# Performance work log

Hardware: AMD Instinct MI355X
Metric: run time of the kernel (lower is better)

The kernel has to match this reference:

```python
import jax, jax.numpy as jnp
import numpy as np

B, N, C, H = 16, 4096, 384, 8
D = C // H  # head_dim = 48
WSTD = 0.02


def setup_inputs() -> dict:
    key = jax.random.key(0)
    ks = jax.random.split(key, 9)
    return {
        "x": jax.random.normal(ks[0], (B, N, C), dtype=jnp.float32),
        "conv_w": jax.random.normal(ks[1], (C, C), dtype=jnp.float32) * WSTD,  # Conv1d k=1, squeezed
        "conv_b": jax.random.normal(ks[2], (C,), dtype=jnp.float32) * WSTD,
        "wq": jax.random.normal(ks[3], (C, C), dtype=jnp.float32) * WSTD,
        "bq": jax.random.normal(ks[4], (C,), dtype=jnp.float32) * WSTD,
        "wkv": jax.random.normal(ks[5], (2 * C, C), dtype=jnp.float32) * WSTD,
        "bkv": jax.random.normal(ks[6], (2 * C,), dtype=jnp.float32) * WSTD,
        "wp": jax.random.normal(ks[7], (C, C), dtype=jnp.float32) * WSTD,
        "bp": jax.random.normal(ks[8], (C,), dtype=jnp.float32) * WSTD,
    }


def reference(x, conv_w, conv_b, wq, bq, wkv, bkv, wp, bp):
    b, n, c = x.shape
    h, d = H, c // H
    # Conv1d kernel_size=1 over channels == per-token linear: y = x @ W^T + b
    x_in = jnp.einsum("bnc,oc->bno", x, conv_w) + conv_b  # [B,N,C]
    # q: reshape(B,N,1,H,d).permute(2,0,3,4,1)[0] -> [B,H,d,N]
    q = (x_in @ wq.T + bq).reshape(b, n, h, d).transpose(0, 2, 3, 1)  # [B,H,d,N]
    kv = (x_in @ wkv.T + bkv).reshape(b, n, 2, h, d).transpose(2, 0, 3, 4, 1)  # [2,B,H,d,N]
    k, v = kv[0], kv[1]
    scale = jnp.asarray(n, x.dtype) ** -0.5  # note: N^-0.5, not head_dim^-0.5
    attn = jax.nn.softmax((q * scale) @ jnp.swapaxes(k, -2, -1), axis=-1)  # [B,H,d,d]
    out = attn @ v  # [B,H,d,N]
    # transpose(1,2) -> [B,d,H,N], then raw reshape to [B,N,C] (verbatim torch layout)
    out = jnp.transpose(out, (0, 2, 1, 3)).reshape(b, n, c)
    return out @ wp.T + bp
```

## Files before the change

### kernel.cpp

```cpp
#include <hip/hip_runtime.h>
#include <hip/hip_bf16.h>
#include <stdint.h>

#define DEVI static __device__ __forceinline__

typedef __attribute__((ext_vector_type(4))) float f32x4;
typedef __attribute__((ext_vector_type(8))) short bf16x8;
typedef unsigned short u16;
typedef unsigned int u32;
typedef unsigned long long u64;

#define BB 16
#define NN 4096
#define CC 384
#define HH 8
#define DD 48

DEVI u16 f2bf(float f) {
  union { float f; u32 u; } c; c.f = f;
  u32 u = c.u;
  u32 r = (u + 0x7FFFu + ((u >> 16) & 1u)) >> 16;
  return (u16)r;
}
DEVI float bf2f(u16 h) {
  union { float f; u32 u; } c; c.u = ((u32)h) << 16;
  return c.f;
}
DEVI void stage8(u16* dst, const float* src) {
  const f32x4 a = *(const f32x4*)(src);
  const f32x4 b = *(const f32x4*)(src + 4);
  union { bf16x8 v; u16 u[8]; } o;
  o.u[0] = f2bf(a[0]); o.u[1] = f2bf(a[1]); o.u[2] = f2bf(a[2]); o.u[3] = f2bf(a[3]);
  o.u[4] = f2bf(b[0]); o.u[5] = f2bf(b[1]); o.u[6] = f2bf(b[2]); o.u[7] = f2bf(b[3]);
  *(bf16x8*)dst = o.v;
}

typedef const __attribute__((address_space(1))) void* gas_ptr;
typedef __attribute__((address_space(3))) void* las_ptr;
DEVI void gload16(const void* g, void* l) {
  __builtin_amdgcn_global_load_lds((gas_ptr)g, (las_ptr)l, 16, 0, 0);
}

__global__ __launch_bounds__(256)
void f32_to_bf16(const float* __restrict__ in, u16* __restrict__ out, int n8) {
  const int i = blockIdx.x * 256 + threadIdx.x;
  if (i >= n8) return;
  u16 tmp[8];
  stage8(tmp, in + (size_t)i * 8);
  *(bf16x8*)(out + (size_t)i * 8) = *(bf16x8*)tmp;
}

__global__ __launch_bounds__(256)
void convert_x(const float* __restrict__ x, u16* __restrict__ xb,
               u16* __restrict__ xbT) {
  __shared__ __align__(8) u16 Lt[64 * 68];
  const int ct = blockIdx.x, nt = blockIdx.y, b = blockIdx.z;
  const int t = threadIdx.x;
  const int n0 = nt * 64, c0 = ct * 64;
#pragma unroll
  for (int it = 0; it < 4; ++it) {
    const int row = it * 16 + (t >> 4), col = (t & 15) * 4;
    const f32x4 v = *(const f32x4*)&x[((size_t)(b * NN + n0 + row)) * CC + c0 + col];
    u64 pk = (u64)f2bf(v[0]) | ((u64)f2bf(v[1]) << 16) |
             ((u64)f2bf(v[2]) << 32) | ((u64)f2bf(v[3]) << 48);
    *(u64*)(&Lt[row * 68 + col]) = pk;
  }
  __syncthreads();
#pragma unroll
  for (int it = 0; it < 2; ++it) {
    const int v = it * 256 + t, row = v >> 3, cg = v & 7;
    union { bf16x8 o; u64 q[2]; } u;
    u.q[0] = *(const u64*)(&Lt[row * 68 + cg * 8]);
    u.q[1] = *(const u64*)(&Lt[row * 68 + cg * 8 + 4]);
    *(bf16x8*)&xb[((size_t)(b * NN + n0 + row)) * CC + c0 + cg * 8] = u.o;
  }
#pragma unroll
  for (int it = 0; it < 2; ++it) {
    const int v = it * 256 + t, c = v >> 3, ng = v & 7;
    union { bf16x8 o; u16 e[8]; } u;
#pragma unroll
    for (int r = 0; r < 8; ++r) u.e[r] = Lt[(ng * 8 + r) * 68 + c];
    *(bf16x8*)&xbT[((size_t)(b * CC + c0 + c)) * NN + n0 + ng * 8] = u.o;
  }
}

__global__ __launch_bounds__(256)
void transpose_cw(const float* __restrict__ cw, u16* __restrict__ cwT) {
  __shared__ __align__(8) u16 Lt[64 * 68];
  const int mt = blockIdx.x, ct = blockIdx.y;
  const int t = threadIdx.x;
  const int m0 = mt * 64, c0 = ct * 64;
#pragma unroll
  for (int it = 0; it < 4; ++it) {
    const int row = it * 16 + (t >> 4), col = (t & 15) * 4;
    const f32x4 v = *(const f32x4*)&cw[(size_t)(m0 + row) * CC + c0 + col];
    u64 pk = (u64)f2bf(v[0]) | ((u64)f2bf(v[1]) << 16) |
             ((u64)f2bf(v[2]) << 32) | ((u64)f2bf(v[3]) << 48);
    *(u64*)(&Lt[row * 68 + col]) = pk;
  }
  __syncthreads();
#pragma unroll
  for (int it = 0; it < 2; ++it) {
    const int v = it * 256 + t, c = v >> 3, mg = v & 7;
    union { bf16x8 o; u16 e[8]; } u;
#pragma unroll
    for (int r = 0; r < 8; ++r) u.e[r] = Lt[(mg * 8 + r) * 68 + c];
    *(bf16x8*)&cwT[(size_t)(c0 + c) * CC + m0 + mg * 8] = u.o;
  }
}

__global__ __launch_bounds__(256)
void bias_fuse(const float* __restrict__ wq, const float* __restrict__ bq,
               const float* __restrict__ wkv, const float* __restrict__ bkv,
               const float* __restrict__ cb, float* __restrict__ bf_) {
  const int o = blockIdx.x * 4 + (threadIdx.x >> 6);
  const int lane = threadIdx.x & 63;
  const float* wrow;
  float b0;
  if (o < CC) { wrow = wq + (size_t)o * CC;        b0 = bq[o]; }
  else        { wrow = wkv + (size_t)(o - CC) * CC; b0 = bkv[o - CC]; }
  float s = 0.f;
  for (int m = lane; m < CC; m += 64) s += wrow[m] * cb[m];
#pragma unroll
  for (int off = 32; off; off >>= 1) s += __shfl_xor(s, off, 64);
  if (lane == 0) bf_[o] = b0 + s;
}

__global__ __launch_bounds__(256)
void colsum(const u16* __restrict__ xbT, float* __restrict__ sx) {
  const int b = blockIdx.y, c = blockIdx.x * 16 + (threadIdx.x >> 4);
  const int sl = threadIdx.x & 15;
  const u16* src = xbT + ((size_t)(b * CC + c)) * NN + sl * 256;
  float s = 0.f;
  for (int i = 0; i < 32; ++i) {
    const bf16x8 v = *(const bf16x8*)(src + i * 8);
#pragma unroll
    for (int r = 0; r < 8; ++r) s += bf2f((u16)v[r]);
  }
#pragma unroll
  for (int m = 1; m < 16; m <<= 1) s += __shfl_xor(s, m, 64);
  if (sl == 0) sx[b * CC + c] = s;
}

__global__ __launch_bounds__(128)
void proj_sx(const u16* __restrict__ Wf, const float* __restrict__ sx,
             float* __restrict__ P) {
  __shared__ float sl[CC];
  const int b = blockIdx.y, o = blockIdx.x * 128 + threadIdx.x;
  for (int i = threadIdx.x; i < CC; i += 128) sl[i] = sx[b * CC + i];
  __syncthreads();
  float acc = 0.f;
  const u16* wr = Wf + (size_t)o * CC;
  for (int c8 = 0; c8 < CC; c8 += 8) {
    const bf16x8 w = *(const bf16x8*)(wr + c8);
#pragma unroll
    for (int r = 0; r < 8; ++r) acc += bf2f((u16)w[r]) * sl[c8 + r];
  }
  P[b * 768 + o] = acc;
}

template<typename OT, int BIASMODE, int TRI = 0, int SWZ = 1>
__global__ __launch_bounds__(256)
void gemm_f(const u16* __restrict__ A, const u16* __restrict__ W,
            const float* __restrict__ bias, OT* __restrict__ C,
            int M, int N, int K, int klen, int nbn, int nbm, int tpb,
            long sA, long sW, long sC, long sCp, long sBias) {
  constexpr int BK = 64;
  __shared__ __align__(16) u16 smem[32768];

  const int nx = gridDim.x;
  const int lin = blockIdx.x;
  const int lin2 = SWZ ? (lin & 7) * (nx >> 3) + (lin >> 3) : lin;
  const int b = lin2 / tpb;
  int t2 = lin2 % tpb;
  int bn, bm, p;
  if constexpr (TRI) {
    const int tl = t2 % 6; p = t2 / 6;
    bm = tl < 3 ? 0 : (tl < 5 ? 1 : 2);
    bn = tl < 3 ? tl : (tl < 5 ? tl - 2 : 2);
  } else {
    bn = t2 % nbn; t2 /= nbn;
    bm = t2 % nbm;
    p = t2 / nbm;
  }
  A += (size_t)b * sA; W += (size_t)b * sW;
  C += (size_t)b * sC + (size_t)p * sCp;
  if (BIASMODE) bias += (size_t)b * sBias;

  const int t = threadIdx.x;
  const int wid = t >> 6, lane = t & 63;
  const int wr = wid >> 1, wc = wid & 1;
  const int row0 = bm * 128, col0 = bn * 128;
  const int lrow = lane & 15;
  const int lswz = (lane & 7) << 3;
  const int kstart = p * klen;

  const int arow = t >> 3;
  const int scol = ((t & 7) ^ ((t >> 3) & 7)) * 8;
  const u16* Ag = A + (size_t)(row0 + arow) * K + scol;
  const u16* Wg = W + (size_t)(col0 + arow) * K + scol;

  f32x4 acc[4][4] = {};
  const int NT = klen >> 6;

  auto stage = [&](int buf, int kt) {
    u16* Al = smem + buf * 16384 + t * 8;
    u16* Bl = smem + buf * 16384 + 8192 + t * 8;
    const int k0 = kstart + kt * BK;
#pragma unroll
    for (int it = 0; it < 4; ++it) {
      gload16(Ag + (size_t)(it * 32) * K + k0, Al + it * 2048);
      gload16(Wg + (size_t)(it * 32) * K + k0, Bl + it * 2048);
    }
  };

  stage(0, 0);
  __syncthreads();
  int cur = 0;
  for (int kt = 0; kt < NT; ++kt) {
    if (kt + 1 < NT) stage(cur ^ 1, kt + 1);
    const u16* As = smem + cur * 16384;
    const u16* Bs = smem + cur * 16384 + 8192;
#pragma unroll
    for (int kk = 0; kk < 2; ++kk) {
      const int lk = (kk * 32 + (lane >> 4) * 8) ^ lswz;
      bf16x8 af[4], bf[4];
#pragma unroll
      for (int i = 0; i < 4; ++i)
        af[i] = *(const bf16x8*)&As[(wr * 64 + i * 16 + lrow) * BK + lk];
#pragma unroll
      for (int j = 0; j < 4; ++j)
        bf[j] = *(const bf16x8*)&Bs[(wc * 64 + j * 16 + lrow) * BK + lk];
#pragma unroll
      for (int i = 0; i < 4; ++i)
#pragma unroll
        for (int j = 0; j < 4; ++j)
          acc[i][j] = __builtin_amdgcn_mfma_f32_16x16x32_bf16(af[i], bf[j], acc[i][j], 0, 0, 0);
    }
    __syncthreads();
    cur ^= 1;
  }

  const int lr = (lane >> 4) * 4;
  if constexpr (sizeof(OT) == 2) {
    u16* Ct = smem;
#pragma unroll
    for (int i = 0; i < 4; ++i)
#pragma unroll
      for (int j = 0; j < 4; ++j) {
        const int ccol = wc * 64 + j * 16 + lrow;
        float bv = 0.f;
        if constexpr (BIASMODE == 1) bv = bias[col0 + ccol];
#pragma unroll
        for (int r = 0; r < 4; ++r) {
          const int rrow = wr * 64 + i * 16 + lr + r;
          float b2 = bv;
          if constexpr (BIASMODE == 2) b2 = bias[row0 + rrow];
          Ct[rrow * 132 + ccol] = f2bf(acc[i][j][r] + b2);
        }
      }
    __syncthreads();
#pragma unroll
    for (int it = 0; it < 8; ++it) {
      const int id = it * 256 + t;
      const int row = id >> 4, c16 = (id & 15) * 8;
      *(bf16x8*)((u16*)C + (size_t)(row0 + row) * N + col0 + c16) =
          *(const bf16x8*)&Ct[row * 132 + c16];
    }
  } else {
    const int orow = row0 + wr * 64, ocol = col0 + wc * 64;
#pragma unroll
    for (int i = 0; i < 4; ++i)
#pragma unroll
      for (int j = 0; j < 4; ++j) {
        const int cc2 = ocol + j * 16 + lrow;
        float bv = 0.f;
        if constexpr (BIASMODE == 1) bv = bias[cc2];
#pragma unroll
        for (int r = 0; r < 4; ++r) {
          const int rr = orow + i * 16 + lr + r;
          float b2 = bv;
          if constexpr (BIASMODE == 2) b2 = bias[rr];
          C[(size_t)rr * N + cc2] = acc[i][j][r] + b2;
        }
      }
  }
}

__global__ __launch_bounds__(256)
void reduceG(const float* __restrict__ Gp, u16* __restrict__ Gbf) {
  const int b = blockIdx.y;
  const int e = blockIdx.x * 256 + threadIdx.x;
  const int i = e / CC, j = e % CC;
  const int ee = (i <= j) ? e : (j * CC + i);
  const float* s = Gp + (size_t)b * 4 * 147456 + ee;
  Gbf[(size_t)b * 147456 + e] =
      f2bf(s[0] + s[147456] + s[2 * 147456] + s[3 * 147456]);
}

__global__ __launch_bounds__(256)
void s_softmax(const u16* __restrict__ M1g, const u16* __restrict__ Wf,
               const float* __restrict__ bf_, const float* __restrict__ P,
               const u16* __restrict__ UvT, u16* __restrict__ AUb,
               float* __restrict__ rbias) {
  __shared__ float Sf[48 * 52];
  __shared__ __align__(16) u16 att[48 * 56];
  const int bh = blockIdx.x, b = bh >> 3, h = bh & 7;
  const int t = threadIdx.x, wid = t >> 6, lane = t & 63;
  const int lrow = lane & 15, lkq = lane >> 4;

  if (wid < 3) {
    f32x4 acc[3] = {};
    const u16* Arow = M1g + (size_t)b * 147456 + (size_t)(h * 48 + wid * 16 + lrow) * CC;
    const u16* Brow = Wf + (size_t)(CC + h * 48) * CC;
    for (int ks = 0; ks < 12; ++ks) {
      const int k = ks * 32 + lkq * 8;
      const bf16x8 af = *(const bf16x8*)(Arow + k);
#pragma unroll
      for (int j = 0; j < 3; ++j) {
        const bf16x8 bfr = *(const bf16x8*)(Brow + (size_t)(j * 16 + lrow) * CC + k);
        acc[j] = __builtin_amdgcn_mfma_f32_16x16x32_bf16(af, bfr, acc[j], 0, 0, 0);
      }
    }
    const int lr = lkq * 4;
#pragma unroll
    for (int j = 0; j < 3; ++j)
#pragma unroll
      for (int r = 0; r < 4; ++r)
        Sf[(wid * 16 + lr + r) * 52 + j * 16 + lrow] = acc[j][r];
  }
  __syncthreads();

  if (t < 48) {
    const float bi = bf_[h * 48 + t];
    const float pq = P[b * 768 + h * 48 + t];
    float row[48];
    float mx = -1e30f;
#pragma unroll
    for (int j = 0; j < 48; ++j) {
      const float g = bf_[CC + h * 48 + j];
      const float pk = P[b * 768 + CC + h * 48 + j];
      const float s = (Sf[t * 52 + j] + bi * pk + pq * g + 4096.f * bi * g) * 0.015625f;
      row[j] = s;
      mx = fmaxf(mx, s);
    }
    float sum = 0.f;
#pragma unroll
    for (int j = 0; j < 48; ++j) { row[j] = __expf(row[j] - mx); sum += row[j]; }
    const float inv = 1.f / sum;
    float rb = 0.f;
#pragma unroll
    for (int j = 0; j < 48; ++j) {
      const float a = row[j] * inv;
      att[t * 56 + j] = f2bf(a);
      rb += a * bf_[2 * CC + h * 48 + j];
    }
#pragma unroll
    for (int j = 48; j < 56; ++j) att[t * 56 + j] = 0;
    rbias[b * CC + t * 8 + h] = rb;
  }
  __syncthreads();

  f32x4 acc[3][6] = {};
  const u16* Vbase = UvT + h * 48;
  const bf16x8 z = {};
#pragma unroll
  for (int kk = 0; kk < 2; ++kk) {
    const int k = kk * 32 + lkq * 8;
    bf16x8 af[3];
#pragma unroll
    for (int i = 0; i < 3; ++i) {
      af[i] = *(const bf16x8*)&att[(i * 16 + lrow) * 56 + k];
      if (k >= 48) af[i] = z;
    }
#pragma unroll
    for (int ct = 0; ct < 6; ++ct) {
      const int c = wid * 96 + ct * 16 + lrow;
      bf16x8 bfr = *(const bf16x8*)(Vbase + (size_t)c * CC + k);
      if (k >= 48) bfr = z;
#pragma unroll
      for (int i = 0; i < 3; ++i)
        acc[i][ct] = __builtin_amdgcn_mfma_f32_16x16x32_bf16(af[i], bfr, acc[i][ct], 0, 0, 0);
    }
  }
  const int lr = lkq * 4;
#pragma unroll
  for (int i = 0; i < 3; ++i)
#pragma unroll
    for (int ct = 0; ct < 6; ++ct) {
      const int c = wid * 96 + ct * 16 + lrow;
#pragma unroll
      for (int r = 0; r < 4; ++r) {
        const int ii = i * 16 + lr + r;
        AUb[(size_t)b * 147456 + (size_t)(ii * 8 + h) * CC + c] = f2bf(acc[i][ct][r]);
      }
    }
}

extern "C" void kernel_launch(void* const* d_in, const int* in_sizes, int n_in,
                              void* d_out, int out_size, void* d_ws, size_t ws_size,
                              hipStream_t stream) {
  const float* x      = (const float*)d_in[0];
  const float* conv_w = (const float*)d_in[1];
  const float* conv_b = (const float*)d_in[2];
  const float* wq     = (const float*)d_in[3];
  const float* bq     = (const float*)d_in[4];
  const float* wkv    = (const float*)d_in[5];
  const float* bkv    = (const float*)d_in[6];
  const float* wp     = (const float*)d_in[7];
  const float* bp     = (const float*)d_in[8];
  float* y = (float*)d_out;

  char* ws = (char*)d_ws;
  u16*   Wf    = (u16*)(ws + 0);
  float* bf_   = (float*)(ws + 884736);
  u16*   wpb   = (u16*)(ws + 889344);
  u16*   UvT   = (u16*)(ws + 1184256);
  float* sx    = (float*)(ws + 1479168);
  float* P     = (float*)(ws + 1503744);
  float* rb    = (float*)(ws + 1552896);
  u16*   M1g   = (u16*)(ws + 1577472);
  u16*   Gbf   = (u16*)(ws + 6296064);
  u16*   AUb   = (u16*)(ws + 11014656);
  float* Gpart = (float*)(ws + 15733248);
  u16*   wtopb = (u16*)(ws + 53481984);
  u16*   cwTb  = (u16*)(ws + 54366720);
  u16*   xb    = (u16*)(ws + 54661632);
  u16*   xbT   = (u16*)(ws + 104993280);
  u16*   R     = xbT;

  convert_x<<<dim3(6, 64, 16), dim3(256), 0, stream>>>(x, xb, xbT);
  f32_to_bf16<<<dim3(72), dim3(256), 0, stream>>>(wp, wpb, (CC * CC) / 8);
  f32_to_bf16<<<dim3(72), dim3(256), 0, stream>>>(wq, wtopb, (CC * CC) / 8);
  f32_to_bf16<<<dim3(144), dim3(256), 0, stream>>>(wkv, wtopb + CC * CC,
                                                   (2 * CC * CC) / 8);
  transpose_cw<<<dim3(6, 6), dim3(256), 0, stream>>>(conv_w, cwTb);
  bias_fuse<<<dim3(288), dim3(256), 0, stream>>>(wq, bq, wkv, bkv, conv_b, bf_);
  gemm_f<u16, 0, 0, 0><<<dim3(18), dim3(256), 0, stream>>>(
      wtopb, cwTb, nullptr, Wf, 2 * CC, CC, CC, CC, 3, 6, 18,
      0, 0, 0, 0, 0);
  gemm_f<u16, 0, 0, 0><<<dim3(9), dim3(256), 0, stream>>>(
      cwTb, wtopb + 2 * CC * CC, nullptr, UvT, CC, CC, CC, CC, 3, 3, 9,
      0, 0, 0, 0, 0);
  colsum<<<dim3(24, 16), dim3(256), 0, stream>>>(xbT, sx);
  proj_sx<<<dim3(6, 16), dim3(128), 0, stream>>>(Wf, sx, P);
  gemm_f<float, 0, 1><<<dim3(384), dim3(256), 0, stream>>>(
      xbT, xbT, nullptr, Gpart, CC, CC, NN, 1024, 3, 3, 24,
      (long)CC * NN, (long)CC * NN, 4L * 147456, 147456, 0);
  reduceG<<<dim3(576, 16), dim3(256), 0, stream>>>(Gpart, Gbf);
  gemm_f<u16, 0><<<dim3(144), dim3(256), 0, stream>>>(
      Wf, Gbf, nullptr, M1g, CC, CC, CC, CC, 3, 3, 9,
      0, 147456, 147456, 0, 0);
  s_softmax<<<dim3(128), dim3(256), 0, stream>>>(M1g, Wf, bf_, P, UvT, AUb, rb);
  gemm_f<u16, 2><<<dim3(1536), dim3(256), 0, stream>>>(
      AUb, xb, rb, R, CC, NN, CC, CC, 32, 3, 96,
      147456, (long)NN * CC, (long)NN * CC, 0, CC);
  gemm_f<float, 1><<<dim3(1536), dim3(256), 0, stream>>>(
      R, wpb, bp, y, BB * NN, CC, CC, CC, 3, 512, 1536,
      0, 0, 0, 0, 0);
}
```

Baseline: 226.1 us.

## Single-buffer GEMM LDS for occupancy and rework transpose kernels via packed u32 LDS

```diff
diff --git a/kernel.cpp b/kernel.cpp
--- a/kernel.cpp
+++ b/kernel.cpp
@@ -53,58 +53,69 @@
 __global__ __launch_bounds__(256)
 void convert_x(const float* __restrict__ x, u16* __restrict__ xb,
                u16* __restrict__ xbT) {
-  __shared__ __align__(8) u16 Lt[64 * 68];
+  __shared__ u32 LtT[64 * 33];
   const int ct = blockIdx.x, nt = blockIdx.y, b = blockIdx.z;
   const int t = threadIdx.x;
   const int n0 = nt * 64, c0 = ct * 64;
-#pragma unroll
-  for (int it = 0; it < 4; ++it) {
-    const int row = it * 16 + (t >> 4), col = (t & 15) * 4;
-    const f32x4 v = *(const f32x4*)&x[((size_t)(b * NN + n0 + row)) * CC + c0 + col];
-    u64 pk = (u64)f2bf(v[0]) | ((u64)f2bf(v[1]) << 16) |
-             ((u64)f2bf(v[2]) << 32) | ((u64)f2bf(v[3]) << 48);
-    *(u64*)(&Lt[row * 68 + col]) = pk;
+  const int cl = (t & 15) * 4;
+  const int np = t >> 4;
+#pragma unroll
+  for (int pass = 0; pass < 2; ++pass) {
+    const int w = np + pass * 16;
+    const int n = w * 2;
+    const float* s0 = &x[((size_t)(b * NN + n0 + n)) * CC + c0 + cl];
+    const f32x4 a = *(const f32x4*)s0;
+    const f32x4 bv = *(const f32x4*)(s0 + CC);
+    const u16 a0 = f2bf(a[0]), a1 = f2bf(a[1]), a2 = f2bf(a[2]), a3 = f2bf(a[3]);
+    const u16 b0 = f2bf(bv[0]), b1 = f2bf(bv[1]), b2 = f2bf(bv[2]), b3 = f2bf(bv[3]);
+    *(u64*)&xb[((size_t)(b * NN + n0 + n)) * CC + c0 + cl] =
+        (u64)a0 | ((u64)a1 << 16) | ((u64)a2 << 32) | ((u64)a3 << 48);
+    *(u64*)&xb[((size_t)(b * NN + n0 + n + 1)) * CC + c0 + cl] =
+        (u64)b0 | ((u64)b1 << 16) | ((u64)b2 << 32) | ((u64)b3 << 48);
+    LtT[(cl + 0) * 33 + w] = (u32)a0 | ((u32)b0 << 16);
+    LtT[(cl + 1) * 33 + w] = (u32)a1 | ((u32)b1 << 16);
+    LtT[(cl + 2) * 33 + w] = (u32)a2 | ((u32)b2 << 16);
+    LtT[(cl + 3) * 33 + w] = (u32)a3 | ((u32)b3 << 16);
   }
   __syncthreads();
 #pragma unroll
-  for (int it = 0; it < 2; ++it) {
-    const int v = it * 256 + t, row = v >> 3, cg = v & 7;
-    union { bf16x8 o; u64 q[2]; } u;
-    u.q[0] = *(const u64*)(&Lt[row * 68 + cg * 8]);
-    u.q[1] = *(const u64*)(&Lt[row * 68 + cg * 8 + 4]);
-    *(bf16x8*)&xb[((size_t)(b * NN + n0 + row)) * CC + c0 + cg * 8] = u.o;
-  }
-#pragma unroll
-  for (int it = 0; it < 2; ++it) {
-    const int v = it * 256 + t, c = v >> 3, ng = v & 7;
-    union { bf16x8 o; u16 e[8]; } u;
-#pragma unroll
-    for (int r = 0; r < 8; ++r) u.e[r] = Lt[(ng * 8 + r) * 68 + c];
+  for (int pass = 0; pass < 2; ++pass) {
+    const int v = pass * 256 + t;
+    const int c = v >> 3, ng = v & 7;
+    union { bf16x8 o; u32 q[4]; } u;
+#pragma unroll
+    for (int r = 0; r < 4; ++r) u.q[r] = LtT[c * 33 + ng * 4 + r];
     *(bf16x8*)&xbT[((size_t)(b * CC + c0 + c)) * NN + n0 + ng * 8] = u.o;
   }
 }
 
 __global__ __launch_bounds__(256)
 void transpose_cw(const float* __restrict__ cw, u16* __restrict__ cwT) {
-  __shared__ __align__(8) u16 Lt[64 * 68];
+  __shared__ u32 LtT[64 * 33];
   const int mt = blockIdx.x, ct = blockIdx.y;
   const int t = threadIdx.x;
   const int m0 = mt * 64, c0 = ct * 64;
-#pragma unroll
-  for (int it = 0; it < 4; ++it) {
-    const int row = it * 16 + (t >> 4), col = (t & 15) * 4;
-    const f32x4 v = *(const f32x4*)&cw[(size_t)(m0 + row) * CC + c0 + col];
-    u64 pk = (u64)f2bf(v[0]) | ((u64)f2bf(v[1]) << 16) |
-             ((u64)f2bf(v[2]) << 32) | ((u64)f2bf(v[3]) << 48);
-    *(u64*)(&Lt[row * 68 + col]) = pk;
+  const int cl = (t & 15) * 4;
+  const int mp = t >> 4;
+#pragma unroll
+  for (int pass = 0; pass < 2; ++pass) {
+    const int w = mp + pass * 16;
+    const int m = w * 2;
+    const float* s0 = &cw[(size_t)(m0 + m) * CC + c0 + cl];
+    const f32x4 a = *(const f32x4*)s0;
+    const f32x4 bv = *(const f32x4*)(s0 + CC);
+#pragma unroll
+    for (int i = 0; i < 4; ++i)
+      LtT[(cl + i) * 33 + w] = (u32)f2bf(a[i]) | ((u32)f2bf(bv[i]) << 16);
   }
   __syncthreads();
 #pragma unroll
-  for (int it = 0; it < 2; ++it) {
-    const int v = it * 256 + t, c = v >> 3, mg = v & 7;
-    union { bf16x8 o; u16 e[8]; } u;
-#pragma unroll
-    for (int r = 0; r < 8; ++r) u.e[r] = Lt[(mg * 8 + r) * 68 + c];
+  for (int pass = 0; pass < 2; ++pass) {
+    const int v = pass * 256 + t;
+    const int c = v >> 3, mg = v & 7;
+    union { bf16x8 o; u32 q[4]; } u;
+#pragma unroll
+    for (int r = 0; r < 4; ++r) u.q[r] = LtT[c * 33 + mg * 4 + r];
     *(bf16x8*)&cwT[(size_t)(c0 + c) * CC + m0 + mg * 8] = u.o;
   }
 }
@@ -166,7 +177,7 @@
             int M, int N, int K, int klen, int nbn, int nbm, int tpb,
             long sA, long sW, long sC, long sCp, long sBias) {
   constexpr int BK = 64;
-  __shared__ __align__(16) u16 smem[32768];
+  __shared__ __align__(16) u16 smem[16896];
 
   const int nx = gridDim.x;
   const int lin = blockIdx.x;
@@ -199,28 +210,23 @@
   const int scol = ((t & 7) ^ ((t >> 3) & 7)) * 8;
   const u16* Ag = A + (size_t)(row0 + arow) * K + scol;
   const u16* Wg = W + (size_t)(col0 + arow) * K + scol;
+  u16* As = smem;
+  u16* Bs = smem + 8192;
 
   f32x4 acc[4][4] = {};
   const int NT = klen >> 6;
 
-  auto stage = [&](int buf, int kt) {
-    u16* Al = smem + buf * 16384 + t * 8;
-    u16* Bl = smem + buf * 16384 + 8192 + t * 8;
+  for (int kt = 0; kt < NT; ++kt) {
+    __syncthreads();
     const int k0 = kstart + kt * BK;
+    u16* Al = As + t * 8;
+    u16* Bl = Bs + t * 8;
 #pragma unroll
     for (int it = 0; it < 4; ++it) {
       gload16(Ag + (size_t)(it * 32) * K + k0, Al + it * 2048);
       gload16(Wg + (size_t)(it * 32) * K + k0, Bl + it * 2048);
     }
-  };
-
-  stage(0, 0);
-  __syncthreads();
-  int cur = 0;
-  for (int kt = 0; kt < NT; ++kt) {
-    if (kt + 1 < NT) stage(cur ^ 1, kt + 1);
-    const u16* As = smem + cur * 16384;
-    const u16* Bs = smem + cur * 16384 + 8192;
+    __syncthreads();
 #pragma unroll
     for (int kk = 0; kk < 2; ++kk) {
       const int lk = (kk * 32 + (lane >> 4) * 8) ^ lswz;
@@ -237,12 +243,11 @@
         for (int j = 0; j < 4; ++j)
           acc[i][j] = __builtin_amdgcn_mfma_f32_16x16x32_bf16(af[i], bf[j], acc[i][j], 0, 0, 0);
     }
-    __syncthreads();
-    cur ^= 1;
   }
 
   const int lr = (lane >> 4) * 4;
   if constexpr (sizeof(OT) == 2) {
+    __syncthreads();
     u16* Ct = smem;
 #pragma unroll
     for (int i = 0; i < 4; ++i)
```

After: 240.4 us. 1.06x slower.
